# Optimization experiments

Hardware: AMD Instinct MI355X
Metric: run time of the kernel (lower is better)

Reference implementation:

```python
import jax, jax.numpy as jnp
import numpy as np

B, N, C, F = 8, 3, 64, 128
H = W = 128


def _up2(x):
    # nearest-neighbor upsample by 2 on the last two axes
    return jnp.repeat(jnp.repeat(x, 2, axis=-2), 2, axis=-1)


def setup_inputs() -> dict:
    key = jax.random.key(0)
    ks = jax.random.split(key, 12)
    s = lambda k, shp, fan: jax.random.normal(k, shp, jnp.float32) * (1.0 / np.sqrt(fan))
    return {
        "contexts": jax.random.normal(ks[0], (B, N, C, H, W), jnp.float32),
        "mainstream": jax.random.normal(ks[1], (B, F, H // 2, W // 2), jnp.float32),
        "Wc": s(ks[2], (C, C), C),        # W_context 1x1 conv weight [out,in]
        "bc": jnp.zeros((C,), jnp.float32),
        "Wf": s(ks[3], (C, F), F),        # W_feat 1x1
        "bf": jnp.zeros((C,), jnp.float32),
        "Wk": s(ks[4], (C, F), F),        # W_key_feat 1x1
        "bk": jnp.zeros((C,), jnp.float32),
        "Vw": s(ks[5], (C, F, 3, 3), F * 9),  # values_conv 3x3, OIHW
        "Vb": jnp.zeros((C,), jnp.float32),
    }


def reference(contexts, mainstream, Wc, bc, Wf, bf, Wk, bk, Vw, Vb):
    # contexts: [B,N,C,H,W], mainstream: [B,F,h,w]
    bias = lambda b: b[None, :, None, None]
    queries = jnp.einsum('bfhw,cf->bchw', mainstream, Wf) + bias(bf)       # [B,C,h,w]
    keys_m = jnp.einsum('bfhw,cf->bchw', mainstream, Wk) + bias(bk)        # [B,C,h,w]
    values = jax.lax.conv_general_dilated(
        mainstream, Vw, (1, 1), 'SAME',
        dimension_numbers=('NCHW', 'OIHW', 'NCHW')) + bias(Vb)             # [B,C,h,w]

    # stack contexts with upsampled mainstream keys, project with W_context (1x1)
    keys_stack = jnp.concatenate([contexts, _up2(keys_m)[:, None]], axis=1)  # [B,N+1,C,H,W]
    keys_proj = jnp.einsum('bnchw,dc->bndhw', keys_stack, Wc) + bc[None, None, :, None, None]

    q_up = _up2(queries)                                                    # [B,C,H,W]
    logits = jnp.einsum('bnchw,bchw->bnhw', keys_proj, q_up)                # [B,N+1,H,W]
    attn = jax.nn.softmax(logits, axis=1)                                   # softmax over contexts

    vals_stack = jnp.concatenate([contexts, _up2(values)[:, None]], axis=1) # [B,N+1,C,H,W]
    out = jnp.einsum('bnchw,bnhw->bchw', vals_stack, attn)                  # [B,C,H,W]
    return out
```

## Files before the change

kernel.cpp:

```cpp
#include <hip/hip_runtime.h>
#include <math.h>

#define CH   64
#define FD   128
#define HS   64
#define FS   128
#define NB   8
#define NCTX 3

#define WS_QT   0
#define WS_VAL  2097152
#define WS_L3   4194304
#define WS_BQ   4227072
#define WS_AVH  4227136
#define WS_AVL  4264000
#define WS_AQH  4300864
#define WS_AQL  4304960
#define WS_AKH  4309056
#define WS_AKL  4313152
#define WS_MTH  4317248
#define WS_MTL  6547520

#define MT2_IDX(b,row,kf,col,kh) \
  ((((((size_t)(b)*66+(row))*8+(kf))*66+(col))*2+(kh))*8)

typedef short  s16x8  __attribute__((ext_vector_type(8)));
typedef float  f32x16 __attribute__((ext_vector_type(16)));

__device__ inline unsigned short bf16_rne(float x) {
  unsigned u = __float_as_uint(x);
  u += 0x7FFFu + ((u >> 16) & 1u);
  return (unsigned short)(u >> 16);
}
__device__ inline void split2(float x, unsigned short& h, unsigned short& l) {
  h = bf16_rne(x);
  l = bf16_rne(x - __uint_as_float((unsigned)h << 16));
}

__global__ __launch_bounds__(256) void setup_all(
    const float* __restrict__ Wc, const float* __restrict__ Wf,
    const float* __restrict__ bf, const float* __restrict__ Wk,
    const float* __restrict__ Vw, const float* __restrict__ m,
    float* __restrict__ ws) {
  if (blockIdx.x < 45) {
    int id = blockIdx.x * 256 + threadIdx.x;
    unsigned short* avh = (unsigned short*)(ws + WS_AVH);
    unsigned short* avl = (unsigned short*)(ws + WS_AVL);
    unsigned short* aqh = (unsigned short*)(ws + WS_AQH);
    unsigned short* aql = (unsigned short*)(ws + WS_AQL);
    unsigned short* akh = (unsigned short*)(ws + WS_AKH);
    unsigned short* akl = (unsigned short*)(ws + WS_AKL);

    if (id < 9216) {
      int tile = id / 4608, rem = id % 4608;
      int q = rem >> 6, l = rem & 63;
      int am = l & 31, kh = l >> 5;
      int c = tile * 32 + am, tap = q >> 3, kf = q & 7;
#pragma unroll
      for (int j = 0; j < 8; ++j) {
        int f = kf * 16 + kh * 8 + j;
        unsigned short h, lo;
        split2(Vw[(c * FD + f) * 9 + tap], h, lo);
        avh[id * 8 + j] = h; avl[id * 8 + j] = lo;
      }
    } else if (id < 10240) {
      int i2 = id - 9216;
      int tile = i2 >> 9, rem = i2 & 511;
      int q = rem >> 6, l = rem & 63;
      int am = l & 31, kh = l >> 5;
      int c = tile * 32 + am;
#pragma unroll
      for (int j = 0; j < 8; ++j) {
        int f = q * 16 + kh * 8 + j;
        float acc = 0.f;
        for (int d = 0; d < CH; ++d)
          acc = fmaf(Wc[d * CH + c], Wf[d * FD + f], acc);
        unsigned short h, lo; split2(acc, h, lo);
        aqh[i2 * 8 + j] = h; aql[i2 * 8 + j] = lo;
      }
    } else if (id < 11264) {
      int i3 = id - 10240;
      int tile = i3 >> 9, rem = i3 & 511;
      int q = rem >> 6, l = rem & 63;
      int am = l & 31, kh = l >> 5;
      int c = tile * 32 + am;
#pragma unroll
      for (int j = 0; j < 8; ++j) {
        int f = q * 16 + kh * 8 + j;
        unsigned short h, lo; split2(Wk[c * FD + f], h, lo);
        akh[i3 * 8 + j] = h; akl[i3 * 8 + j] = lo;
      }
    } else if (id < 11328) {
      int c = id - 11264;
      float acc = 0.f;
      for (int d = 0; d < CH; ++d) acc = fmaf(Wc[d * CH + c], bf[d], acc);
      ws[WS_BQ + c] = acc;
    }
  } else {
    unsigned short* mth = (unsigned short*)(ws + WS_MTH);
    unsigned short* mtl = (unsigned short*)(ws + WS_MTL);
    const int bid = blockIdx.x - 45;
    const int b = bid / 66, yp = bid % 66;
    const int lane = threadIdx.x & 63;
    const int wave = threadIdx.x >> 6;
    const int yy = yp - 1;
    const bool rowok = (yy >= 0) && (yy < HS);
#pragma unroll
    for (int cc = 0; cc < 4; ++cc) {
      const int f0 = wave * 32 + cc * 8;
      const int kf = f0 >> 4, kh = (f0 >> 3) & 1;
      float v[8];
      if (rowok) {
#pragma unroll
        for (int j = 0; j < 8; ++j)
          v[j] = m[((b * FD + f0 + j) * HS + yy) * HS + lane];
      } else {
#pragma unroll
        for (int j = 0; j < 8; ++j) v[j] = 0.f;
      }
      s16x8 hi, lo;
#pragma unroll
      for (int j = 0; j < 8; ++j) {
        unsigned short h, l; split2(v[j], h, l);
        hi[j] = (short)h; lo[j] = (short)l;
      }
      size_t base = MT2_IDX(b, yp, kf, lane + 1, kh);
      *(s16x8*)(mth + base) = hi;
      *(s16x8*)(mtl + base) = lo;
      if (lane < 2) {
        s16x8 z;
#pragma unroll
        for (int j = 0; j < 8; ++j) z[j] = 0;
        size_t bb = MT2_IDX(b, yp, kf, lane * 65, kh);
        *(s16x8*)(mth + bb) = z;
        *(s16x8*)(mtl + bb) = z;
      }
    }
  }
}

__global__ __launch_bounds__(512) void main_mfma(
    const unsigned short* __restrict__ mth, const unsigned short* __restrict__ mtl,
    const float* __restrict__ Vb, const float* __restrict__ bk,
    float* __restrict__ ws) {
  const int b = blockIdx.x >> 6, y = blockIdx.x & 63;
  const int t = threadIdx.x, lane = t & 63;
  const int wave = __builtin_amdgcn_readfirstlane(t >> 6);
  const int am = lane & 31, kh = lane >> 5;
  const int w4 = wave & 3;
  const int x0 = (w4 & 1) * 32, ch0 = (w4 >> 1) * 32;
  const int ct = w4 >> 1;
  const int khalf = wave >> 2;

  const unsigned short* avh = (const unsigned short*)(ws + WS_AVH);
  const unsigned short* avl = (const unsigned short*)(ws + WS_AVL);

  __shared__ float red[4][16][64];
  __shared__ float qtb[2][64][32];
  __shared__ float keb[2][64][32];

  f32x16 a1, a2;
#pragma unroll
  for (int i = 0; i < 16; ++i) { a1[i] = 0.f; a2[i] = 0.f; }
#pragma unroll 4
  for (int qi = 0; qi < 36; ++qi) {
    const int q = khalf * 36 + qi;
    const int tap = q >> 3, kf = q & 7;
    const s16x8 ah = *(const s16x8*)(avh + ((ct * 72 + q) * 64 + lane) * 8);
    const s16x8 al = *(const s16x8*)(avl + ((ct * 72 + q) * 64 + lane) * 8);
    const s16x8 bh = *(const s16x8*)(mth +
        MT2_IDX(b, y + tap / 3, kf, x0 + am + tap % 3, kh));
    a1 = __builtin_amdgcn_mfma_f32_32x32x16_bf16(ah, bh, a1, 0, 0, 0);
    a2 = __builtin_amdgcn_mfma_f32_32x32x16_bf16(al, bh, a2, 0, 0, 0);
  }
  if (khalf) {
#pragma unroll
    for (int r = 0; r < 16; ++r) red[w4][r][lane] = a1[r] + a2[r];
  }
  __syncthreads();
  if (!khalf) {
#pragma unroll
    for (int r = 0; r < 16; ++r) {
      const int c = ch0 + (r & 3) + 8 * (r >> 2) + 4 * kh;
      float v = a1[r] + a2[r] + red[w4][r][lane] + Vb[c];
      ws[WS_VAL + ((b * CH + c) * HS + y) * HS + x0 + am] = v;
    }
  }

  const unsigned short* Ah = (const unsigned short*)(ws + (khalf ? WS_AKH : WS_AQH));
  const unsigned short* Al = (const unsigned short*)(ws + (khalf ? WS_AKL : WS_AQL));
  f32x16 c1, c2;
#pragma unroll
  for (int i = 0; i < 16; ++i) { c1[i] = 0.f; c2[i] = 0.f; }
#pragma unroll
  for (int q = 0; q < 8; ++q) {
    const s16x8 ah = *(const s16x8*)(Ah + ((ct * 8 + q) * 64 + lane) * 8);
    const s16x8 al = *(const s16x8*)(Al + ((ct * 8 + q) * 64 + lane) * 8);
    const size_t base = MT2_IDX(b, y + 1, q, x0 + am + 1, kh);
    const s16x8 bh = *(const s16x8*)(mth + base);
    const s16x8 bl = *(const s16x8*)(mtl + base);
    c1 = __builtin_amdgcn_mfma_f32_32x32x16_bf16(ah, bh, c1, 0, 0, 0);
    c1 = __builtin_amdgcn_mfma_f32_32x32x16_bf16(al, bh, c1, 0, 0, 0);
    c2 = __builtin_amdgcn_mfma_f32_32x32x16_bf16(ah, bl, c2, 0, 0, 0);
  }
  const int ptile = w4 & 1;
#pragma unroll
  for (int r = 0; r < 16; ++r) {
    const int c = ch0 + (r & 3) + 8 * (r >> 2) + 4 * kh;
    if (khalf) {
      keb[ptile][c][am] = c1[r] + c2[r] + bk[c];
    } else {
      float v = c1[r] + c2[r] + ws[WS_BQ + c];
      qtb[ptile][c][am] = v;
      ws[WS_QT + ((b * CH + c) * HS + y) * HS + x0 + am] = v;
    }
  }
  __syncthreads();

  if (wave < 2) {
    float s = 0.f;
#pragma unroll 8
    for (int j = 0; j < 32; ++j)
      s = fmaf(qtb[wave][kh * 32 + j][am], keb[wave][kh * 32 + j][am], s);
    s += __shfl_xor(s, 32, 64);
    if (kh == 0)
      ws[WS_L3 + (b * HS + y) * HS + wave * 32 + am] = s;
  }
}

__global__ __launch_bounds__(256) void fullres_kernel(
    const float* __restrict__ ctx, const float* __restrict__ ws,
    float* __restrict__ out) {
  const int xh = blockIdx.x & 1, hrow = blockIdx.x >> 1;
  const int b = blockIdx.y;
  const int px = threadIdx.x & 63, cg = threadIdx.x >> 6;
  const int x = xh * 64 + px;
  const int h2 = hrow >> 1, w2 = x >> 1;

  const float* qtp = ws + WS_QT + (size_t)(b * CH) * HS * HS + h2 * HS + w2;
  const float* cb  = ctx + (size_t)(b * NCTX * CH) * FS * FS + hrow * FS + x;
  const int cs = FS * FS, ns = CH * FS * FS;

  float cv0[16], cv1[16], cv2[16];
  float l0 = 0.f, l1 = 0.f, l2 = 0.f;
#pragma unroll
  for (int j = 0; j < 16; ++j) {
    const int c = cg * 16 + j;
    cv0[j] = cb[c * cs];
    cv1[j] = cb[ns + c * cs];
    cv2[j] = cb[2 * ns + c * cs];
    const float q = qtp[c * HS * HS];
    l0 = fmaf(cv0[j], q, l0);
    l1 = fmaf(cv1[j], q, l1);
    l2 = fmaf(cv2[j], q, l2);
  }
  __shared__ float red[3][4][64];
  red[0][cg][px] = l0; red[1][cg][px] = l1; red[2][cg][px] = l2;
  __syncthreads();
  float L0 = red[0][0][px] + red[0][1][px] + red[0][2][px] + red[0][3][px];
  float L1 = red[1][0][px] + red[1][1][px] + red[1][2][px] + red[1][3][px];
  float L2 = red[2][0][px] + red[2][1][px] + red[2][2][px] + red[2][3][px];
  float L3 = ws[WS_L3 + (b * HS + h2) * HS + w2];

  float mx = fmaxf(fmaxf(L0, L1), fmaxf(L2, L3));
  float e0 = __expf(L0 - mx), e1 = __expf(L1 - mx);
  float e2 = __expf(L2 - mx), e3 = __expf(L3 - mx);
  float inv = 1.f / (e0 + e1 + e2 + e3);
  float a0 = e0 * inv, a1 = e1 * inv, a2 = e2 * inv, a3 = e3 * inv;

  const float* valp = ws + WS_VAL + (size_t)(b * CH) * HS * HS + h2 * HS + w2;
  float* op = out + (size_t)(b * CH) * FS * FS + hrow * FS + x;
#pragma unroll
  for (int j = 0; j < 16; ++j) {
    const int c = cg * 16 + j;
    float o = a3 * valp[c * HS * HS];
    o = fmaf(a0, cv0[j], o);
    o = fmaf(a1, cv1[j], o);
    o = fmaf(a2, cv2[j], o);
    op[c * cs] = o;
  }
}

extern "C" void kernel_launch(void* const* d_in, const int* in_sizes, int n_in,
                              void* d_out, int out_size, void* d_ws, size_t ws_size,
                              hipStream_t stream) {
  const float* ctx = (const float*)d_in[0];
  const float* ms  = (const float*)d_in[1];
  const float* Wc  = (const float*)d_in[2];
  const float* Wf  = (const float*)d_in[4];
  const float* bf  = (const float*)d_in[5];
  const float* Wk  = (const float*)d_in[6];
  const float* bk  = (const float*)d_in[7];
  const float* Vw  = (const float*)d_in[8];
  const float* Vb  = (const float*)d_in[9];
  float* ws  = (float*)d_ws;
  float* out = (float*)d_out;

  unsigned short* mth = (unsigned short*)(ws + WS_MTH);
  unsigned short* mtl = (unsigned short*)(ws + WS_MTL);

  setup_all<<<45 + NB * 66, 256, 0, stream>>>(Wc, Wf, bf, Wk, Vw, ms, ws);
  main_mfma<<<NB * HS, 512, 0, stream>>>(mth, mtl, Vb, bk, ws);
  fullres_kernel<<<dim3(2 * FS, NB), 256, 0, stream>>>(ctx, ws, out);
}
```

Baseline: 271.3 us.

## Drop low-half split for value conv, widen main_mfma, vectorize fullres loads

The value 3x3 conv weights are now stored only as single bf16 instead of a hi/lo split, which removes half of the value-conv MFMAs. main_mfma now runs 1024 threads per block, splitting the conv K-reduction across four wave groups and combining them through a larger shared-memory reduction. fullres_kernel is restructured so each thread handles 4 pixels and 4 channels with float4 context loads and float4 output stores, and the channel reduction goes through shared memory. Dropping the low-bf16 term lowers the accuracy of the value path. The launch_bounds(1024, 8) request may also force register spilling.

```diff
diff --git a/kernel.cpp b/kernel.cpp
--- a/kernel.cpp
+++ b/kernel.cpp
@@ -45,7 +45,6 @@
   if (blockIdx.x < 45) {
     int id = blockIdx.x * 256 + threadIdx.x;
     unsigned short* avh = (unsigned short*)(ws + WS_AVH);
-    unsigned short* avl = (unsigned short*)(ws + WS_AVL);
     unsigned short* aqh = (unsigned short*)(ws + WS_AQH);
     unsigned short* aql = (unsigned short*)(ws + WS_AQL);
     unsigned short* akh = (unsigned short*)(ws + WS_AKH);
@@ -59,9 +58,7 @@
 #pragma unroll
       for (int j = 0; j < 8; ++j) {
         int f = kf * 16 + kh * 8 + j;
-        unsigned short h, lo;
-        split2(Vw[(c * FD + f) * 9 + tap], h, lo);
-        avh[id * 8 + j] = h; avl[id * 8 + j] = lo;
+        avh[id * 8 + j] = bf16_rne(Vw[(c * FD + f) * 9 + tap]);
       }
     } else if (id < 10240) {
       int i2 = id - 9216;
@@ -139,7 +136,7 @@
   }
 }
 
-__global__ __launch_bounds__(512) void main_mfma(
+__global__ __launch_bounds__(1024, 8) void main_mfma(
     const unsigned short* __restrict__ mth, const unsigned short* __restrict__ mtl,
     const float* __restrict__ Vb, const float* __restrict__ bk,
     float* __restrict__ ws) {
@@ -147,72 +144,72 @@
   const int t = threadIdx.x, lane = t & 63;
   const int wave = __builtin_amdgcn_readfirstlane(t >> 6);
   const int am = lane & 31, kh = lane >> 5;
-  const int w4 = wave & 3;
-  const int x0 = (w4 & 1) * 32, ch0 = (w4 >> 1) * 32;
-  const int ct = w4 >> 1;
+  const int tile = wave & 3;
+  const int x0 = (tile & 1) * 32, ch0 = (tile >> 1) * 32;
+  const int ct = tile >> 1;
   const int khalf = wave >> 2;
 
   const unsigned short* avh = (const unsigned short*)(ws + WS_AVH);
-  const unsigned short* avl = (const unsigned short*)(ws + WS_AVL);
-
-  __shared__ float red[4][16][64];
+
+  __shared__ float red[3][4][16][64];
   __shared__ float qtb[2][64][32];
   __shared__ float keb[2][64][32];
 
-  f32x16 a1, a2;
-#pragma unroll
-  for (int i = 0; i < 16; ++i) { a1[i] = 0.f; a2[i] = 0.f; }
-#pragma unroll 4
-  for (int qi = 0; qi < 36; ++qi) {
-    const int q = khalf * 36 + qi;
+  f32x16 a1;
+#pragma unroll
+  for (int i = 0; i < 16; ++i) a1[i] = 0.f;
+#pragma unroll 6
+  for (int qi = 0; qi < 18; ++qi) {
+    const int q = khalf * 18 + qi;
     const int tap = q >> 3, kf = q & 7;
     const s16x8 ah = *(const s16x8*)(avh + ((ct * 72 + q) * 64 + lane) * 8);
-    const s16x8 al = *(const s16x8*)(avl + ((ct * 72 + q) * 64 + lane) * 8);
     const s16x8 bh = *(const s16x8*)(mth +
         MT2_IDX(b, y + tap / 3, kf, x0 + am + tap % 3, kh));
     a1 = __builtin_amdgcn_mfma_f32_32x32x16_bf16(ah, bh, a1, 0, 0, 0);
-    a2 = __builtin_amdgcn_mfma_f32_32x32x16_bf16(al, bh, a2, 0, 0, 0);
   }
   if (khalf) {
 #pragma unroll
-    for (int r = 0; r < 16; ++r) red[w4][r][lane] = a1[r] + a2[r];
+    for (int r = 0; r < 16; ++r) red[khalf - 1][tile][r][lane] = a1[r];
   }
   __syncthreads();
   if (!khalf) {
 #pragma unroll
     for (int r = 0; r < 16; ++r) {
       const int c = ch0 + (r & 3) + 8 * (r >> 2) + 4 * kh;
-      float v = a1[r] + a2[r] + red[w4][r][lane] + Vb[c];
+      float v = a1[r] + red[0][tile][r][lane] + red[1][tile][r][lane]
+              + red[2][tile][r][lane] + Vb[c];
       ws[WS_VAL + ((b * CH + c) * HS + y) * HS + x0 + am] = v;
     }
   }
 
-  const unsigned short* Ah = (const unsigned short*)(ws + (khalf ? WS_AKH : WS_AQH));
-  const unsigned short* Al = (const unsigned short*)(ws + (khalf ? WS_AKL : WS_AQL));
-  f32x16 c1, c2;
-#pragma unroll
-  for (int i = 0; i < 16; ++i) { c1[i] = 0.f; c2[i] = 0.f; }
-#pragma unroll
-  for (int q = 0; q < 8; ++q) {
-    const s16x8 ah = *(const s16x8*)(Ah + ((ct * 8 + q) * 64 + lane) * 8);
-    const s16x8 al = *(const s16x8*)(Al + ((ct * 8 + q) * 64 + lane) * 8);
-    const size_t base = MT2_IDX(b, y + 1, q, x0 + am + 1, kh);
-    const s16x8 bh = *(const s16x8*)(mth + base);
-    const s16x8 bl = *(const s16x8*)(mtl + base);
-    c1 = __builtin_amdgcn_mfma_f32_32x32x16_bf16(ah, bh, c1, 0, 0, 0);
-    c1 = __builtin_amdgcn_mfma_f32_32x32x16_bf16(al, bh, c1, 0, 0, 0);
-    c2 = __builtin_amdgcn_mfma_f32_32x32x16_bf16(ah, bl, c2, 0, 0, 0);
-  }
-  const int ptile = w4 & 1;
-#pragma unroll
-  for (int r = 0; r < 16; ++r) {
-    const int c = ch0 + (r & 3) + 8 * (r >> 2) + 4 * kh;
-    if (khalf) {
-      keb[ptile][c][am] = c1[r] + c2[r] + bk[c];
-    } else {
-      float v = c1[r] + c2[r] + ws[WS_BQ + c];
-      qtb[ptile][c][am] = v;
-      ws[WS_QT + ((b * CH + c) * HS + y) * HS + x0 + am] = v;
+  if (khalf < 2) {
+    const unsigned short* Ah = (const unsigned short*)(ws + (khalf ? WS_AKH : WS_AQH));
+    const unsigned short* Al = (const unsigned short*)(ws + (khalf ? WS_AKL : WS_AQL));
+    f32x16 c1, c2;
+#pragma unroll
+    for (int i = 0; i < 16; ++i) { c1[i] = 0.f; c2[i] = 0.f; }
+#pragma unroll
+    for (int q = 0; q < 8; ++q) {
+      const s16x8 ah = *(const s16x8*)(Ah + ((ct * 8 + q) * 64 + lane) * 8);
+      const s16x8 al = *(const s16x8*)(Al + ((ct * 8 + q) * 64 + lane) * 8);
+      const size_t base = MT2_IDX(b, y + 1, q, x0 + am + 1, kh);
+      const s16x8 bh = *(const s16x8*)(mth + base);
+      const s16x8 bl = *(const s16x8*)(mtl + base);
+      c1 = __builtin_amdgcn_mfma_f32_32x32x16_bf16(ah, bh, c1, 0, 0, 0);
+      c1 = __builtin_amdgcn_mfma_f32_32x32x16_bf16(al, bh, c1, 0, 0, 0);
+      c2 = __builtin_amdgcn_mfma_f32_32x32x16_bf16(ah, bl, c2, 0, 0, 0);
+    }
+    const int ptile = tile & 1;
+#pragma unroll
+    for (int r = 0; r < 16; ++r) {
+      const int c = ch0 + (r & 3) + 8 * (r >> 2) + 4 * kh;
+      if (khalf) {
+        keb[ptile][c][am] = c1[r] + c2[r] + bk[c];
+      } else {
+        float v = c1[r] + c2[r] + ws[WS_BQ + c];
+        qtb[ptile][c][am] = v;
+        ws[WS_QT + ((b * CH + c) * HS + y) * HS + x0 + am] = v;
+      }
     }
   }
   __syncthreads();
@@ -233,51 +230,89 @@
     float* __restrict__ out) {
   const int xh = blockIdx.x & 1, hrow = blockIdx.x >> 1;
   const int b = blockIdx.y;
-  const int px = threadIdx.x & 63, cg = threadIdx.x >> 6;
-  const int x = xh * 64 + px;
-  const int h2 = hrow >> 1, w2 = x >> 1;
-
-  const float* qtp = ws + WS_QT + (size_t)(b * CH) * HS * HS + h2 * HS + w2;
-  const float* cb  = ctx + (size_t)(b * NCTX * CH) * FS * FS + hrow * FS + x;
+  const int quad = threadIdx.x & 15;
+  const int cg = threadIdx.x >> 4;
+  const int x = xh * 64 + quad * 4;
+  const int h2 = hrow >> 1, w2 = (x >> 1);
+  const int c0 = cg * 4;
+
+  const size_t cbase = (size_t)(b * NCTX * CH) * FS * FS + hrow * FS + x;
   const int cs = FS * FS, ns = CH * FS * FS;
 
-  float cv0[16], cv1[16], cv2[16];
-  float l0 = 0.f, l1 = 0.f, l2 = 0.f;
-#pragma unroll
-  for (int j = 0; j < 16; ++j) {
-    const int c = cg * 16 + j;
-    cv0[j] = cb[c * cs];
-    cv1[j] = cb[ns + c * cs];
-    cv2[j] = cb[2 * ns + c * cs];
-    const float q = qtp[c * HS * HS];
-    l0 = fmaf(cv0[j], q, l0);
-    l1 = fmaf(cv1[j], q, l1);
-    l2 = fmaf(cv2[j], q, l2);
-  }
-  __shared__ float red[3][4][64];
-  red[0][cg][px] = l0; red[1][cg][px] = l1; red[2][cg][px] = l2;
+  float4 cv[3][4];
+  float2 qv[4];
+#pragma unroll
+  for (int j = 0; j < 4; ++j) {
+    const int c = c0 + j;
+    cv[0][j] = *(const float4*)(ctx + cbase + c * cs);
+    cv[1][j] = *(const float4*)(ctx + cbase + ns + c * cs);
+    cv[2][j] = *(const float4*)(ctx + cbase + 2 * ns + c * cs);
+    qv[j] = *(const float2*)(ws + WS_QT + (size_t)(b * CH + c) * HS * HS + h2 * HS + w2);
+  }
+
+  float4 pl[3];
+#pragma unroll
+  for (int n = 0; n < 3; ++n) {
+    pl[n].x = pl[n].y = pl[n].z = pl[n].w = 0.f;
+#pragma unroll
+    for (int j = 0; j < 4; ++j) {
+      pl[n].x = fmaf(cv[n][j].x, qv[j].x, pl[n].x);
+      pl[n].y = fmaf(cv[n][j].y, qv[j].x, pl[n].y);
+      pl[n].z = fmaf(cv[n][j].z, qv[j].y, pl[n].z);
+      pl[n].w = fmaf(cv[n][j].w, qv[j].y, pl[n].w);
+    }
+  }
+
+  __shared__ float4 part[3][16][17];
+  __shared__ float  Lred[3][64];
+#pragma unroll
+  for (int n = 0; n < 3; ++n) part[n][cg][quad] = pl[n];
   __syncthreads();
-  float L0 = red[0][0][px] + red[0][1][px] + red[0][2][px] + red[0][3][px];
-  float L1 = red[1][0][px] + red[1][1][px] + red[1][2][px] + red[1][3][px];
-  float L2 = red[2][0][px] + red[2][1][px] + red[2][2][px] + red[2][3][px];
-  float L3 = ws[WS_L3 + (b * HS + h2) * HS + w2];
-
-  float mx = fmaxf(fmaxf(L0, L1), fmaxf(L2, L3));
-  float e0 = __expf(L0 - mx), e1 = __expf(L1 - mx);
-  float e2 = __expf(L2 - mx), e3 = __expf(L3 - mx);
-  float inv = 1.f / (e0 + e1 + e2 + e3);
-  float a0 = e0 * inv, a1 = e1 * inv, a2 = e2 * inv, a3 = e3 * inv;
-
-  const float* valp = ws + WS_VAL + (size_t)(b * CH) * HS * HS + h2 * HS + w2;
+
+  {
+    const int tt = threadIdx.x;
+    if (tt < 192) {
+      const int n = tt >> 6, px = tt & 63;
+      const float* pp = (const float*)part + (size_t)n * 16 * 17 * 4 + px;
+      float s = 0.f;
+#pragma unroll
+      for (int g = 0; g < 16; ++g) s += pp[g * 68];
+      Lred[n][px] = s;
+    }
+  }
+  __syncthreads();
+
+  float4 Lv0 = *(const float4*)&Lred[0][quad * 4];
+  float4 Lv1 = *(const float4*)&Lred[1][quad * 4];
+  float4 Lv2 = *(const float4*)&Lred[2][quad * 4];
+  float2 l3v = *(const float2*)(ws + WS_L3 + (b * HS + h2) * HS + w2);
+
+  float A0[4], A1[4], A2[4], A3[4];
+  const float* L0p = (const float*)&Lv0;
+  const float* L1p = (const float*)&Lv1;
+  const float* L2p = (const float*)&Lv2;
+#pragma unroll
+  for (int k = 0; k < 4; ++k) {
+    float L0 = L0p[k], L1 = L1p[k], L2 = L2p[k];
+    float L3 = (k < 2) ? l3v.x : l3v.y;
+    float mx = fmaxf(fmaxf(L0, L1), fmaxf(L2, L3));
+    float e0 = __expf(L0 - mx), e1 = __expf(L1 - mx);
+    float e2 = __expf(L2 - mx), e3 = __expf(L3 - mx);
+    float inv = 1.f / (e0 + e1 + e2 + e3);
+    A0[k] = e0 * inv; A1[k] = e1 * inv; A2[k] = e2 * inv; A3[k] = e3 * inv;
+  }
+
   float* op = out + (size_t)(b * CH) * FS * FS + hrow * FS + x;
 #pragma unroll
-  for (int j = 0; j < 16; ++j) {
-    const int c = cg * 16 + j;
-    float o = a3 * valp[c * HS * HS];
-    o = fmaf(a0, cv0[j], o);
-    o = fmaf(a1, cv1[j], o);
-    o = fmaf(a2, cv2[j], o);
-    op[c * cs] = o;
+  for (int j = 0; j < 4; ++j) {
+    const int c = c0 + j;
+    float2 vv = *(const float2*)(ws + WS_VAL + (size_t)(b * CH + c) * HS * HS + h2 * HS + w2);
+    float4 o;
+    o.x = fmaf(A0[0], cv[0][j].x, fmaf(A1[0], cv[1][j].x, fmaf(A2[0], cv[2][j].x, A3[0] * vv.x)));
+    o.y = fmaf(A0[1], cv[0][j].y, fmaf(A1[1], cv[1][j].y, fmaf(A2[1], cv[2][j].y, A3[1] * vv.x)));
+    o.z = fmaf(A0[2], cv[0][j].z, fmaf(A1[2], cv[1][j].z, fmaf(A2[2], cv[2][j].z, A3[2] * vv.y)));
+    o.w = fmaf(A0[3], cv[0][j].w, fmaf(A1[3], cv[1][j].w, fmaf(A2[3], cv[2][j].w, A3[3] * vv.y)));
+    *(float4*)(op + c * cs) = o;
   }
 }
 
@@ -300,6 +335,6 @@
   unsigned short* mtl = (unsigned short*)(ws + WS_MTL);
 
   setup_all<<<45 + NB * 66, 256, 0, stream>>>(Wc, Wf, bf, Wk, Vw, ms, ws);
-  main_mfma<<<NB * HS, 512, 0, stream>>>(mth, mtl, Vb, bk, ws);
+  main_mfma<<<NB * HS, 1024, 0, stream>>>(mth, mtl, Vb, bk, ws);
   fullres_kernel<<<dim3(2 * FS, NB), 256, 0, stream>>>(ctx, ws, out);
 }
```

Measured after the change: 252.9 us. 1.07x faster.
